# Optimization experiments

Hardware: AMD Instinct MI355X
Metric: run time of the kernel (lower is better)

The kernel has to match this reference:

```python
import jax, jax.numpy as jnp
import numpy as np

N = 50000        # nodes
DEG = 16         # fixed out-degree per row (CSR)
E = N * DEG      # edges
H = 4            # attention heads
D = 32           # head feature dim
NEG_SLOPE = 0.2  # GAT leaky-relu slope (scalar hyperparam from forward args)


def setup_inputs() -> dict:
    key = jax.random.key(0)
    k1, k2, k3, k4 = jax.random.split(key, 4)
    attn_row = jax.random.normal(k1, (N, H), dtype=jnp.float32)   # a_dst . Wh_i per head
    attn_col = jax.random.normal(k2, (N, H), dtype=jnp.float32)   # a_src . Wh_j per head
    in_feat = jax.random.normal(k3, (N, H, D), dtype=jnp.float32)  # transformed node feats
    col_indices = jax.random.randint(k4, (E,), 0, N, dtype=jnp.int32)
    row_indptr = (jnp.arange(N + 1, dtype=jnp.int32) * DEG)        # CSR pointers, fixed degree
    return {
        "attn_row": attn_row,
        "attn_col": attn_col,
        "in_feat": in_feat,
        "row_indptr": row_indptr,
        "col_indices": col_indices,
    }


def reference(attn_row, attn_col, in_feat, row_indptr, col_indices):
    # Fused GAT: per-edge score = leaky_relu(attn_row[i] + attn_col[j]),
    # softmax over each destination row's edges, then weighted sparse aggregation.
    n = attn_row.shape[0]
    e = col_indices.shape[0]
    # row id of each edge from CSR indptr (jit-safe, static edge count)
    row_ids = jnp.searchsorted(row_indptr, jnp.arange(e, dtype=row_indptr.dtype), side="right") - 1
    score = jax.nn.leaky_relu(attn_row[row_ids] + attn_col[col_indices], NEG_SLOPE)  # [E,H]
    # numerically-stable edge softmax per destination row
    m = jax.ops.segment_max(score, row_ids, num_segments=n)        # [N,H]
    ex = jnp.exp(score - m[row_ids])                               # [E,H]
    denom = jax.ops.segment_sum(ex, row_ids, num_segments=n)       # [N,H]
    alpha = ex / denom[row_ids]                                    # [E,H]
    # gather neighbor features, weight, scatter-add to destinations
    msg = alpha[:, :, None] * in_feat[col_indices]                 # [E,H,D]
    out = jax.ops.segment_sum(msg, row_ids, num_segments=n)        # [N,H,D]
    return out
```

## Files before the change

### kernel.cpp

```cpp
#include <hip/hip_runtime.h>
#include <hip/hip_fp16.h>
#include <math.h>


#define GAT_H 4
#define GAT_D 32
#define GAT_DEG 16
#define GAT_NEG_SLOPE 0.2f

struct alignas(8) half4 { __half2 lo, hi; };
typedef float floatx4 __attribute__((ext_vector_type(4)));

__global__ __launch_bounds__(256) void gat_cvt_kernel(
    const floatx4* __restrict__ in, half4* __restrict__ outp, int n4)
{
    const int t = blockIdx.x * 256 + threadIdx.x;
    if (t < n4) {
        const floatx4 v = __builtin_nontemporal_load(&in[t]);
        half4 o;
        o.lo = __floats2half2_rn(v.x, v.y);
        o.hi = __floats2half2_rn(v.z, v.w);
        outp[t] = o;
    }
}

template <bool FP16>
__global__ __launch_bounds__(256, 4) void gat_main_kernel(
    const float*   __restrict__ attn_row,
    const float*   __restrict__ attn_col,
    const float2*  __restrict__ feat32,
    const __half2* __restrict__ feat16,
    const int*     __restrict__ row_indptr,
    const int*     __restrict__ col_indices,
    float*         __restrict__ out,
    int n)
{
    const int wave_id = (int)((blockIdx.x * (unsigned)blockDim.x + threadIdx.x) >> 6);
    const int lane    = threadIdx.x & 63;
    if (wave_id >= n) return;
    const int dst = wave_id;
    const int h   = lane >> 4;
    const int q   = lane & 15;

    int start = row_indptr[dst];
    const int deg = row_indptr[dst + 1] - start;
    start = __builtin_amdgcn_readfirstlane(start);

    int idx[GAT_DEG];
    {
        const int4* cip = reinterpret_cast<const int4*>(col_indices + start);
        #pragma unroll
        for (int p = 0; p < 4; ++p) {
            const int4 c = cip[p];
            idx[4*p+0] = c.x; idx[4*p+1] = c.y;
            idx[4*p+2] = c.z; idx[4*p+3] = c.w;
        }
    }

    const float ac = attn_col[idx[q] * GAT_H + h];
    const float ar = attn_row[dst * GAT_H + h];

    __half2 hv[GAT_DEG];
    float2  fv[GAT_DEG];
    #pragma unroll
    for (int k = 0; k < GAT_DEG; ++k) {
        const size_t off = (size_t)idx[k] * (GAT_H * GAT_D / 2) + h * 16 + q;
        if (FP16) hv[k] = feat16[off];
        else      fv[k] = feat32[off];
    }

    float s = -INFINITY;
    if (q < deg) {
        const float x = ar + ac;
        s = (x > 0.0f) ? x : GAT_NEG_SLOPE * x;
    }
    float m = s;
    #pragma unroll
    for (int off = 1; off < 16; off <<= 1)
        m = fmaxf(m, __shfl_xor(m, off));

    const float ex = (q < deg) ? __expf(s - m) : 0.0f;

    float den = ex;
    #pragma unroll
    for (int off = 1; off < 16; off <<= 1)
        den += __shfl_xor(den, off);
    const float rden = __builtin_amdgcn_rcpf(den);

    const int base = lane & 48;
    float accx = 0.0f, accy = 0.0f;
    #pragma unroll
    for (int k = 0; k < GAT_DEG; ++k) {
        const float a  = __shfl(ex, base + k);
        const float2 f = FP16 ? __half22float2(hv[k]) : fv[k];
        accx = fmaf(a, f.x, accx);
        accy = fmaf(a, f.y, accy);
    }

    union { float2 f2; double d; } r;
    r.f2 = make_float2(accx * rden, accy * rden);
    double* optr = reinterpret_cast<double*>(out) +
                   ((size_t)dst * GAT_H + h) * 16 + q;
    __builtin_nontemporal_store(r.d, optr);
}

extern "C" void kernel_launch(void* const* d_in, const int* in_sizes, int n_in,
                              void* d_out, int out_size, void* d_ws, size_t ws_size,
                              hipStream_t stream) {
    const float* attn_row    = (const float*)d_in[0];
    const float* attn_col    = (const float*)d_in[1];
    const float* in_feat     = (const float*)d_in[2];
    const int*   row_indptr  = (const int*)d_in[3];
    const int*   col_indices = (const int*)d_in[4];
    float*       out         = (float*)d_out;

    const int n      = in_sizes[0] / GAT_H;
    const int n_feat = in_sizes[2];

    const int threads = 256;
    const int blocks  = (n + 3) / 4;

    const size_t fp16_bytes = (size_t)n_feat * sizeof(__half);
    if (ws_size >= fp16_bytes) {
        half4* feat_h = (half4*)d_ws;
        const int n4 = n_feat / 4;
        gat_cvt_kernel<<<(n4 + 255) / 256, 256, 0, stream>>>(
            (const floatx4*)in_feat, feat_h, n4);
        gat_main_kernel<true><<<blocks, threads, 0, stream>>>(
            attn_row, attn_col, (const float2*)in_feat, (const __half2*)feat_h,
            row_indptr, col_indices, out, n);
    } else {
        gat_main_kernel<false><<<blocks, threads, 0, stream>>>(
            attn_row, attn_col, (const float2*)in_feat, (const __half2*)nullptr,
            row_indptr, col_indices, out, n);
    }
}
```

Before: 117.3 us.

## Split fp16 features by head pair and pin each half to an XCD group

The conversion kernel now writes the fp16 features as two planes, one per head pair (heads 0-1 and heads 2-3). The main kernel assigns blocks so that XCDs 0-3 handle one plane and XCDs 4-7 the other, which halves the feature working set each XCD's L2 sees and aims to improve cache hit rate for the random gathers. Each wave now processes one head pair for a node: the 16 neighbours are split across the two half-waves and the partial sums are combined with a cross-half shuffle. The cost is twice as many blocks, with the row indices and attention scores loaded twice per node. The mapping also relies on blocks being dispatched round-robin across the 8 XCDs.

Measured after the change: 196.8 us. +67.8%, slower.

```diff
diff --git a/kernel.cpp b/kernel.cpp
--- a/kernel.cpp
+++ b/kernel.cpp
@@ -12,7 +12,7 @@
 typedef float floatx4 __attribute__((ext_vector_type(4)));
 
 __global__ __launch_bounds__(256) void gat_cvt_kernel(
-    const floatx4* __restrict__ in, half4* __restrict__ outp, int n4)
+    const floatx4* __restrict__ in, half4* __restrict__ outp, int n4, int N)
 {
     const int t = blockIdx.x * 256 + threadIdx.x;
     if (t < n4) {
@@ -20,7 +20,9 @@
         half4 o;
         o.lo = __floats2half2_rn(v.x, v.y);
         o.hi = __floats2half2_rn(v.z, v.w);
-        outp[t] = o;
+        const int d4 = t & 7, h = (t >> 3) & 3, nn = t >> 5;
+        const int p = h >> 1, hh = h & 1;
+        outp[((size_t)p * N + nn) * 16 + hh * 8 + d4] = o;
     }
 }
 
@@ -33,53 +35,67 @@
     const int*     __restrict__ row_indptr,
     const int*     __restrict__ col_indices,
     float*         __restrict__ out,
-    int n)
+    int n, int nchunk)
 {
-    const int wave_id = (int)((blockIdx.x * (unsigned)blockDim.x + threadIdx.x) >> 6);
-    const int lane    = threadIdx.x & 63;
-    if (wave_id >= n) return;
-    const int dst = wave_id;
-    const int h   = lane >> 4;
-    const int q   = lane & 15;
+    const int bid = blockIdx.x;
+    const int xcd = bid & 7;
+    const int p   = xcd >> 2;
+    const int j   = (bid >> 3) * 4 + (xcd & 3);
+    if (j >= nchunk) return;
+
+    const int lane = threadIdx.x & 63;
+    const int wid  = threadIdx.x >> 6;
+    const int dst  = j * 4 + wid;
+    if (dst >= n) return;
 
     int start = row_indptr[dst];
     const int deg = row_indptr[dst + 1] - start;
     start = __builtin_amdgcn_readfirstlane(start);
 
+    const int e  = lane & 15;
+    const int hh = (lane >> 4) & 1;
+    const int hg = 2 * p + hh;
+    int   mycol  = 0;
+    float s      = -INFINITY;
+    if (e < deg) {
+        mycol = col_indices[start + e];
+        const float x = attn_row[dst * GAT_H + hg]
+                      + attn_col[mycol * GAT_H + hg];
+        s = (x > 0.0f) ? x : GAT_NEG_SLOPE * x;
+    }
+
     int idx[GAT_DEG];
     {
         const int4* cip = reinterpret_cast<const int4*>(col_indices + start);
         #pragma unroll
-        for (int p = 0; p < 4; ++p) {
-            const int4 c = cip[p];
-            idx[4*p+0] = c.x; idx[4*p+1] = c.y;
-            idx[4*p+2] = c.z; idx[4*p+3] = c.w;
+        for (int q = 0; q < 4; ++q) {
+            const int4 c4 = cip[q];
+            idx[4*q+0] = c4.x; idx[4*q+1] = c4.y;
+            idx[4*q+2] = c4.z; idx[4*q+3] = c4.w;
         }
     }
 
-    const float ac = attn_col[idx[q] * GAT_H + h];
-    const float ar = attn_row[dst * GAT_H + h];
-
-    __half2 hv[GAT_DEG];
-    float2  fv[GAT_DEG];
+    const int ke = lane >> 5;
+    const int c  = lane & 31;
+    __half2 hv[8];
+    float2  fv[8];
     #pragma unroll
-    for (int k = 0; k < GAT_DEG; ++k) {
-        const size_t off = (size_t)idx[k] * (GAT_H * GAT_D / 2) + h * 16 + q;
-        if (FP16) hv[k] = feat16[off];
-        else      fv[k] = feat32[off];
+    for (int kk = 0; kk < 8; ++kk) {
+        const int src = ke ? idx[2*kk+1] : idx[2*kk];
+        if (FP16) {
+            hv[kk] = feat16[((size_t)p * n + src) * 32 + c];
+        } else {
+            const int hh2 = c >> 4, q2 = c & 15;
+            fv[kk] = feat32[((size_t)src * GAT_H + 2*p + hh2) * 16 + q2];
+        }
     }
 
-    float s = -INFINITY;
-    if (q < deg) {
-        const float x = ar + ac;
-        s = (x > 0.0f) ? x : GAT_NEG_SLOPE * x;
-    }
     float m = s;
     #pragma unroll
     for (int off = 1; off < 16; off <<= 1)
         m = fmaxf(m, __shfl_xor(m, off));
 
-    const float ex = (q < deg) ? __expf(s - m) : 0.0f;
+    const float ex = (e < deg) ? __expf(s - m) : 0.0f;
 
     float den = ex;
     #pragma unroll
@@ -87,21 +103,24 @@
         den += __shfl_xor(den, off);
     const float rden = __builtin_amdgcn_rcpf(den);
 
-    const int base = lane & 48;
     float accx = 0.0f, accy = 0.0f;
     #pragma unroll
-    for (int k = 0; k < GAT_DEG; ++k) {
-        const float a  = __shfl(ex, base + k);
-        const float2 f = FP16 ? __half22float2(hv[k]) : fv[k];
+    for (int kk = 0; kk < 8; ++kk) {
+        const float a  = __shfl(ex, (c >> 4) * 16 + (2*kk + ke));
+        const float2 f = FP16 ? __half22float2(hv[kk]) : fv[kk];
         accx = fmaf(a, f.x, accx);
         accy = fmaf(a, f.y, accy);
     }
+    accx += __shfl_xor(accx, 32);
+    accy += __shfl_xor(accy, 32);
 
-    union { float2 f2; double d; } r;
-    r.f2 = make_float2(accx * rden, accy * rden);
-    double* optr = reinterpret_cast<double*>(out) +
-                   ((size_t)dst * GAT_H + h) * 16 + q;
-    __builtin_nontemporal_store(r.d, optr);
+    if (ke == 0) {
+        union { float2 f2; double d; } r;
+        r.f2 = make_float2(accx * rden, accy * rden);
+        double* optr = reinterpret_cast<double*>(out) +
+                       ((size_t)dst * GAT_H + 2*p + (c >> 4)) * 16 + (c & 15);
+        __builtin_nontemporal_store(r.d, optr);
+    }
 }
 
 extern "C" void kernel_launch(void* const* d_in, const int* in_sizes, int n_in,
@@ -117,21 +136,21 @@
     const int n      = in_sizes[0] / GAT_H;
     const int n_feat = in_sizes[2];
 
-    const int threads = 256;
-    const int blocks  = (n + 3) / 4;
+    const int nchunk = (n + 3) / 4;
+    const int blocks = ((nchunk + 3) / 4) * 8;
 
     const size_t fp16_bytes = (size_t)n_feat * sizeof(__half);
     if (ws_size >= fp16_bytes) {
         half4* feat_h = (half4*)d_ws;
         const int n4 = n_feat / 4;
         gat_cvt_kernel<<<(n4 + 255) / 256, 256, 0, stream>>>(
-            (const floatx4*)in_feat, feat_h, n4);
-        gat_main_kernel<true><<<blocks, threads, 0, stream>>>(
+            (const floatx4*)in_feat, feat_h, n4, n);
+        gat_main_kernel<true><<<blocks, 256, 0, stream>>>(
             attn_row, attn_col, (const float2*)in_feat, (const __half2*)feat_h,
-            row_indptr, col_indices, out, n);
+            row_indptr, col_indices, out, n, nchunk);
     } else {
-        gat_main_kernel<false><<<blocks, threads, 0, stream>>>(
+        gat_main_kernel<false><<<blocks, 256, 0, stream>>>(
             attn_row, attn_col, (const float2*)in_feat, (const __half2*)nullptr,
-            row_indptr, col_indices, out, n);
+            row_indptr, col_indices, out, n, nchunk);
     }
 }
```
